# Optimization experiments

Measured on AMD Instinct MI355X. Metric: run time of the kernel, lower is better.

Reference implementation:

```python
import jax, jax.numpy as jnp
import numpy as np

N_NODES = 50000
N_EDGES = 800000
IN_FEATS = 64
HID_FEATS = 64


def _sage_conv(x, src, dst, W_self, W_neigh, b):
    # mean aggregation over in-neighbors (messages flow src -> dst)
    msg_sum = jax.ops.segment_sum(x[src], dst, num_segments=N_NODES)  # [N, d]
    deg = jax.ops.segment_sum(jnp.ones((src.shape[0],), x.dtype), dst,
                              num_segments=N_NODES)  # [N]
    h_neigh = msg_sum / jnp.maximum(deg, 1.0)[:, None]  # zero-degree nodes -> 0
    return x @ W_self + h_neigh @ W_neigh + b


def setup_inputs() -> dict:
    key = jax.random.key(0)
    ks = jax.random.split(key, 12)
    inputs = jax.random.normal(ks[0], (N_NODES, IN_FEATS), dtype=jnp.float32)
    src = jax.random.randint(ks[1], (N_EDGES,), 0, N_NODES, dtype=jnp.int32)
    dst = jax.random.randint(ks[2], (N_EDGES,), 0, N_NODES, dtype=jnp.int32)

    def glorot(k, shape):
        lim = float(np.sqrt(6.0 / (shape[0] + shape[1])))
        return jax.random.uniform(k, shape, jnp.float32, -lim, lim)

    return {
        "inputs": inputs, "src": src, "dst": dst,
        "W_self1": glorot(ks[3], (IN_FEATS, HID_FEATS)),
        "W_neigh1": glorot(ks[4], (IN_FEATS, HID_FEATS)),
        "b1": jnp.zeros((HID_FEATS,), jnp.float32),
        "W_self2": glorot(ks[5], (HID_FEATS, HID_FEATS)),
        "W_neigh2": glorot(ks[6], (HID_FEATS, HID_FEATS)),
        "b2": jnp.zeros((HID_FEATS,), jnp.float32),
        "W_self3": glorot(ks[7], (HID_FEATS, 1)),
        "W_neigh3": glorot(ks[8], (HID_FEATS, 1)),
        "b3": jnp.zeros((1,), jnp.float32),
    }


def reference(inputs, src, dst,
              W_self1, W_neigh1, b1,
              W_self2, W_neigh2, b2,
              W_self3, W_neigh3, b3):
    h = jax.nn.relu(_sage_conv(inputs, src, dst, W_self1, W_neigh1, b1))
    h = jax.nn.relu(_sage_conv(h, src, dst, W_self2, W_neigh2, b2))
    h = _sage_conv(h, src, dst, W_self3, W_neigh3, b3)
    return h  # [N_NODES, 1]
```

## Files before the change

kernel.cpp:

```cpp
#include <hip/hip_runtime.h>

#define N_NODES 50000
#define N_EDGES 800000
#define F 64
#define NTILES (N_NODES / 16)

#define BNODES 128
#define NB ((N_NODES + BNODES - 1) / BNODES)
#define BCAP 2560
#define EPB 2048
#define SCHUNKS ((N_EDGES + EPB - 1) / EPB)
#define SGRID 512
#define SBLOCK 512
#define PREP_ELEMS (4 * F * F + N_NODES * 16)

typedef __attribute__((ext_vector_type(8))) short short8;
typedef __attribute__((ext_vector_type(4))) float f32x4;

union frag16 { uint4 u; short8 s; };


__device__ __forceinline__ float bflo(unsigned int u) {
    union { unsigned int i; float f; } c; c.i = u << 16; return c.f;
}
__device__ __forceinline__ float bfhi(unsigned int u) {
    union { unsigned int i; float f; } c; c.i = u & 0xFFFF0000u; return c.f;
}
__device__ __forceinline__ unsigned short f2bf(float f) {
    union { float f; unsigned int i; } c; c.f = f;
    unsigned int r = c.i + 0x7FFF + ((c.i >> 16) & 1);
    return (unsigned short)(r >> 16);
}


__global__ __launch_bounds__(SBLOCK) void scatter_prep(
        const int* __restrict__ src, const int* __restrict__ dst,
        int* __restrict__ bcur, unsigned int* __restrict__ binned,
        const float* __restrict__ W0, const float* __restrict__ W1,
        const float* __restrict__ W2, const float* __restrict__ W3,
        unsigned short* __restrict__ Wt,
        const float4* __restrict__ xin, ushort4* __restrict__ xout) {
    __shared__ int lcnt[NB];
    __shared__ int scan[SBLOCK];
    __shared__ int gbase[NB];
    __shared__ int lcur[NB];
    __shared__ unsigned int staged[EPB];

    int tid = threadIdx.x;
    int blk = blockIdx.x;

    for (int idx = blk * SBLOCK + tid; idx < PREP_ELEMS; idx += SGRID * SBLOCK) {
        if (idx < 4 * F * F) {
            int m = idx >> 12;
            int e = idx & 4095;
            int n = e >> 6, k = e & 63;
            const float* W = (m == 0) ? W0 : (m == 1) ? W1 : (m == 2) ? W2 : W3;
            Wt[m * F * F + n * F + k] = f2bf(W[k * F + n]);
        } else {
            int i = idx - 4 * F * F;
            float4 v = xin[i];
            ushort4 o;
            o.x = f2bf(v.x); o.y = f2bf(v.y); o.z = f2bf(v.z); o.w = f2bf(v.w);
            xout[i] = o;
        }
    }

    if (blk >= SCHUNKS) return;

    int e0 = blk * EPB;
    int e1 = min(N_EDGES, e0 + EPB);
    for (int i = tid; i < NB; i += SBLOCK) lcnt[i] = 0;
    __syncthreads();

    int dreg[4], sreg[4];
    #pragma unroll
    for (int t = 0; t < 4; ++t) {
        int i = e0 + tid + t * SBLOCK;
        if (i < e1) { dreg[t] = dst[i]; sreg[t] = src[i]; }
        else        { dreg[t] = -1;     sreg[t] = 0; }
    }
    #pragma unroll
    for (int t = 0; t < 4; ++t)
        if (dreg[t] >= 0) atomicAdd(&lcnt[dreg[t] >> 7], 1);
    __syncthreads();

    int v = (tid < NB) ? lcnt[tid] : 0;
    scan[tid] = v;
    __syncthreads();
    for (int off = 1; off < SBLOCK; off <<= 1) {
        int t2 = (tid >= off) ? scan[tid - off] : 0;
        __syncthreads();
        scan[tid] += t2;
        __syncthreads();
    }
    if (tid < NB) {
        int excl = scan[tid] - v;
        int resv = (v > 0) ? atomicAdd(&bcur[tid], v) : 0;
        gbase[tid] = tid * BCAP + resv - excl;
        lcur[tid] = excl;
    }
    __syncthreads();

    #pragma unroll
    for (int t = 0; t < 4; ++t) {
        if (dreg[t] >= 0) {
            int d = dreg[t];
            int b = d >> 7;
            int dl = d & 127;
            int posl = atomicAdd(&lcur[b], 1);
            staged[posl] = (unsigned)sreg[t] | ((unsigned)dl << 16) | ((unsigned)b << 23);
        }
    }
    __syncthreads();

    int cnt = e1 - e0;
    for (int i = tid; i < cnt; i += SBLOCK) {
        unsigned pk = staged[i];
        binned[gbase[pk >> 23] + i] = pk;
    }
}


__global__ __launch_bounds__(512) void bucket_build(
        const unsigned int* __restrict__ binned, const int* __restrict__ bcur,
        int* __restrict__ row_beg, unsigned short* __restrict__ degs,
        unsigned short* __restrict__ csr16) {
    __shared__ int ncnt[BNODES];
    __shared__ int nofs[BNODES];
    __shared__ int ncur[BNODES];
    int blk = blockIdx.x;
    int tid = threadIdx.x;
    int start = blk * BCAP;
    int cnt = min(bcur[blk], BCAP);

    for (int i = tid; i < BNODES; i += 512) ncnt[i] = 0;
    __syncthreads();

    unsigned preg[5];
    #pragma unroll
    for (int t = 0; t < 5; ++t) {
        int i = tid + t * 512;
        preg[t] = (i < cnt) ? binned[start + i] : 0xFFFFFFFFu;
    }
    #pragma unroll
    for (int t = 0; t < 5; ++t)
        if (preg[t] != 0xFFFFFFFFu)
            atomicAdd(&ncnt[(preg[t] >> 16) & 127], 1);
    __syncthreads();

    if (tid < BNODES) nofs[tid] = ncnt[tid];
    __syncthreads();
    for (int off = 1; off < BNODES; off <<= 1) {
        int t2 = (tid >= off && tid < BNODES) ? nofs[tid - off] : 0;
        __syncthreads();
        if (tid < BNODES) nofs[tid] += t2;
        __syncthreads();
    }
    if (tid < BNODES) {
        int excl = nofs[tid] - ncnt[tid];
        ncur[tid] = excl;
        int node = blk * BNODES + tid;
        row_beg[node] = start + excl;
        degs[node] = (unsigned short)ncnt[tid];
    }
    __syncthreads();

    #pragma unroll
    for (int t = 0; t < 5; ++t) {
        if (preg[t] != 0xFFFFFFFFu) {
            unsigned pk = preg[t];
            int dl = (pk >> 16) & 127;
            int pos = start + atomicAdd(&ncur[dl], 1);
            csr16[pos] = (unsigned short)(pk & 0xFFFF);
        }
    }
}


template <bool PROJ>
__global__ __launch_bounds__(256) void aggtf_kernel(
        const uint4* __restrict__ xh8, const int* __restrict__ row_beg,
        const unsigned short* __restrict__ degs,
        const unsigned short* __restrict__ csr16,
        const uint4* __restrict__ Wst, const uint4* __restrict__ Wnt,
        const float* __restrict__ b, unsigned short* __restrict__ out_bf,
        const float* __restrict__ Ws3, const float* __restrict__ Wn3,
        float* __restrict__ pout, float* __restrict__ qout) {
    __shared__ uint4 lagg[16 * 8];
    int tid  = threadIdx.x;
    int wave = tid >> 6;
    int lane = tid & 63;
    int base = blockIdx.x * 16;

    int g   = lane >> 3;
    int sub = lane & 7;

    int rb_l = 0, dg_l = 0;
    if (lane < 16) { rb_l = row_beg[base + lane]; dg_l = degs[base + lane]; }

    for (int nl = wave * 4; nl < wave * 4 + 4; ++nl) {
        int beg = __shfl(rb_l, nl);
        int deg = __shfl(dg_l, nl);
        int end = beg + deg;
        float a0[8], a1[8];
        #pragma unroll
        for (int j = 0; j < 8; ++j) { a0[j] = 0.f; a1[j] = 0.f; }
        int i = beg + g;
        for (; i + 8 < end; i += 16) {
            int i0 = csr16[i];
            int i1 = csr16[i + 8];
            uint4 v0 = xh8[i0 * 8 + sub];
            uint4 v1 = xh8[i1 * 8 + sub];
            a0[0] += bflo(v0.x); a0[1] += bfhi(v0.x); a0[2] += bflo(v0.y); a0[3] += bfhi(v0.y);
            a0[4] += bflo(v0.z); a0[5] += bfhi(v0.z); a0[6] += bflo(v0.w); a0[7] += bfhi(v0.w);
            a1[0] += bflo(v1.x); a1[1] += bfhi(v1.x); a1[2] += bflo(v1.y); a1[3] += bfhi(v1.y);
            a1[4] += bflo(v1.z); a1[5] += bfhi(v1.z); a1[6] += bflo(v1.w); a1[7] += bfhi(v1.w);
        }
        if (i < end) {
            uint4 v0 = xh8[csr16[i] * 8 + sub];
            a0[0] += bflo(v0.x); a0[1] += bfhi(v0.x); a0[2] += bflo(v0.y); a0[3] += bfhi(v0.y);
            a0[4] += bflo(v0.z); a0[5] += bfhi(v0.z); a0[6] += bflo(v0.w); a0[7] += bfhi(v0.w);
        }
        float s[8];
        #pragma unroll
        for (int j = 0; j < 8; ++j) s[j] = a0[j] + a1[j];
        #pragma unroll
        for (int off = 8; off <= 32; off <<= 1)
            #pragma unroll
            for (int j = 0; j < 8; ++j)
                s[j] += __shfl_xor(s[j], off);
        if (g == 0) {
            float inv = (deg > 0) ? (1.0f / (float)deg) : 0.f;
            unsigned short o[8];
            #pragma unroll
            for (int j = 0; j < 8; ++j) o[j] = f2bf(s[j] * inv);
            uint4 pk;
            pk.x = (unsigned)o[0] | ((unsigned)o[1] << 16);
            pk.y = (unsigned)o[2] | ((unsigned)o[3] << 16);
            pk.z = (unsigned)o[4] | ((unsigned)o[5] << 16);
            pk.w = (unsigned)o[6] | ((unsigned)o[7] << 16);
            lagg[nl * 8 + sub] = pk;
        }
    }
    __syncthreads();
    if (wave != 0) return;

    int lo = lane & 15, hi = lane >> 4;

    frag16 ws[2][4], wn[2][4];
    #pragma unroll
    for (int kt = 0; kt < 2; ++kt)
        #pragma unroll
        for (int jt = 0; jt < 4; ++jt) {
            int n = jt * 16 + lo;
            ws[kt][jt].u = Wst[n * 8 + kt * 4 + hi];
            wn[kt][jt].u = Wnt[n * 8 + kt * 4 + hi];
        }
    float bias_s[4];
    #pragma unroll
    for (int jt = 0; jt < 4; ++jt) bias_s[jt] = b[jt * 16 + lo];
    float w3n_s[4], w3s_s[4];
    if constexpr (PROJ) {
        #pragma unroll
        for (int jt = 0; jt < 4; ++jt) {
            w3n_s[jt] = Wn3[jt * 16 + lo];
            w3s_s[jt] = Ws3[jt * 16 + lo];
        }
    }

    frag16 ax[2], aa[2];
    #pragma unroll
    for (int kt = 0; kt < 2; ++kt) {
        ax[kt].u = xh8[(base + lo) * 8 + kt * 4 + hi];
        aa[kt].u = lagg[lo * 8 + kt * 4 + hi];
    }

    f32x4 acc[4];
    #pragma unroll
    for (int jt = 0; jt < 4; ++jt)
        acc[jt] = f32x4{bias_s[jt], bias_s[jt], bias_s[jt], bias_s[jt]};

    #pragma unroll
    for (int kt = 0; kt < 2; ++kt)
        #pragma unroll
        for (int jt = 0; jt < 4; ++jt) {
            acc[jt] = __builtin_amdgcn_mfma_f32_16x16x32_bf16(ax[kt].s, ws[kt][jt].s, acc[jt], 0, 0, 0);
            acc[jt] = __builtin_amdgcn_mfma_f32_16x16x32_bf16(aa[kt].s, wn[kt][jt].s, acc[jt], 0, 0, 0);
        }

    if constexpr (!PROJ) {
        #pragma unroll
        for (int jt = 0; jt < 4; ++jt)
            #pragma unroll
            for (int r = 0; r < 4; ++r) {
                float h = fmaxf(acc[jt][r], 0.f);
                out_bf[(base + hi * 4 + r) * F + jt * 16 + lo] = f2bf(h);
            }
    } else {
        #pragma unroll
        for (int r = 0; r < 4; ++r) {
            float pr = 0.f, qr = 0.f;
            #pragma unroll
            for (int jt = 0; jt < 4; ++jt) {
                float h = fmaxf(acc[jt][r], 0.f);
                pr += h * w3n_s[jt];
                qr += h * w3s_s[jt];
            }
            #pragma unroll
            for (int off = 1; off < 16; off <<= 1) {
                pr += __shfl_xor(pr, off);
                qr += __shfl_xor(qr, off);
            }
            if (lo == 0) {
                pout[base + hi * 4 + r] = pr;
                qout[base + hi * 4 + r] = qr;
            }
        }
    }
}


__global__ __launch_bounds__(256) void final_kernel(
        const int* __restrict__ row_beg, const unsigned short* __restrict__ degs,
        const unsigned short* __restrict__ csr16,
        const float* __restrict__ p, const float* __restrict__ q,
        const float* __restrict__ b3, float* __restrict__ out, int n_nodes) {
    int grp = threadIdx.x >> 4;
    int ln  = threadIdx.x & 15;
    int node = blockIdx.x * 16 + grp;
    if (node >= n_nodes) return;
    int beg = row_beg[node];
    int deg = degs[node];
    int end = beg + deg;
    float s = 0.f;
    for (int i = beg + ln; i < end; i += 16) s += p[csr16[i]];
    #pragma unroll
    for (int off = 1; off < 16; off <<= 1) s += __shfl_xor(s, off);
    if (ln == 0) {
        float inv = (deg > 0) ? (1.0f / (float)deg) : 0.f;
        out[node] = q[node] + s * inv + b3[0];
    }
}


extern "C" void kernel_launch(void* const* d_in, const int* in_sizes, int n_in,
                              void* d_out, int out_size, void* d_ws, size_t ws_size,
                              hipStream_t stream) {
    const float* x   = (const float*)d_in[0];
    const int*   src = (const int*)d_in[1];
    const int*   dst = (const int*)d_in[2];
    const float* Ws1 = (const float*)d_in[3];
    const float* Wn1 = (const float*)d_in[4];
    const float* b1  = (const float*)d_in[5];
    const float* Ws2 = (const float*)d_in[6];
    const float* Wn2 = (const float*)d_in[7];
    const float* b2  = (const float*)d_in[8];
    const float* Ws3 = (const float*)d_in[9];
    const float* Wn3 = (const float*)d_in[10];
    const float* b3  = (const float*)d_in[11];
    float* out = (float*)d_out;

    char* ws = (char*)d_ws;
    size_t cur = 0;
    auto alloc = [&](size_t bytes) -> void* {
        void* ptr = ws + cur;
        cur += (bytes + 255) & ~(size_t)255;
        return ptr;
    };

    int*            bcur     = (int*)  alloc(NB * sizeof(int));
    unsigned int*   binned   = (unsigned int*)alloc((size_t)NB * BCAP * sizeof(unsigned int));
    int*            row_beg  = (int*)  alloc((size_t)(NB * BNODES) * sizeof(int));
    unsigned short* degs     = (unsigned short*)alloc((size_t)(NB * BNODES) * sizeof(unsigned short));
    unsigned short* csr16    = (unsigned short*)alloc((size_t)NB * BCAP * sizeof(unsigned short));
    unsigned short* xh       = (unsigned short*)alloc((size_t)N_NODES * F * 2);
    unsigned short* h1h      = (unsigned short*)alloc((size_t)N_NODES * F * 2);
    unsigned short* Wt       = (unsigned short*)alloc(4 * F * F * 2);
    float*          p        = (float*)alloc(N_NODES * sizeof(float));
    float*          q        = (float*)alloc(N_NODES * sizeof(float));

    unsigned short* Wst1 = Wt;
    unsigned short* Wnt1 = Wt + F * F;
    unsigned short* Wst2 = Wt + 2 * F * F;
    unsigned short* Wnt2 = Wt + 3 * F * F;

    (void)hipMemsetAsync(bcur, 0, NB * sizeof(int), stream);
    scatter_prep<<<SGRID, SBLOCK, 0, stream>>>(
        src, dst, bcur, binned, Ws1, Wn1, Ws2, Wn2, Wt, (const float4*)x, (ushort4*)xh);
    bucket_build<<<NB, 512, 0, stream>>>(binned, bcur, row_beg, degs, csr16);

    aggtf_kernel<false><<<NTILES, 256, 0, stream>>>(
        (const uint4*)xh, row_beg, degs, csr16,
        (const uint4*)Wst1, (const uint4*)Wnt1, b1, h1h,
        nullptr, nullptr, nullptr, nullptr);
    aggtf_kernel<true><<<NTILES, 256, 0, stream>>>(
        (const uint4*)h1h, row_beg, degs, csr16,
        (const uint4*)Wst2, (const uint4*)Wnt2, b2, nullptr,
        Ws3, Wn3, p, q);
    final_kernel<<<(N_NODES + 15) / 16, 256, 0, stream>>>(
        row_beg, degs, csr16, p, q, b3, out, N_NODES);
}
```

Before: 167.9 us.

## Assign one node per 8-lane group in aggregation, 32 nodes per block

The gather-aggregate phase is remapped. Each 8-lane group now walks one node's full edge list on its own, so a 256-thread block covers 32 nodes, where before a wave spread each node's edges across all 8 groups and then did cross-lane shuffle reductions. This removes the shuffle reductions and the sequential per-wave node loop, and two waves then run the MFMA transform on 16-node halves. The trade-off is a longer serial dependence chain per lane and divergence from uneven degrees within a wave.

```diff
diff --git a/kernel.cpp b/kernel.cpp
--- a/kernel.cpp
+++ b/kernel.cpp
@@ -4,6 +4,7 @@
 #define N_EDGES 800000
 #define F 64
 #define NTILES (N_NODES / 16)
+#define ATILES ((N_NODES + 31) / 32)
 
 #define BNODES 128
 #define NB ((N_NODES + BNODES - 1) / BNODES)
@@ -186,64 +187,62 @@
         const float* __restrict__ b, unsigned short* __restrict__ out_bf,
         const float* __restrict__ Ws3, const float* __restrict__ Wn3,
         float* __restrict__ pout, float* __restrict__ qout) {
-    __shared__ uint4 lagg[16 * 8];
+    __shared__ uint4 lagg[32 * 8];
     int tid  = threadIdx.x;
     int wave = tid >> 6;
     int lane = tid & 63;
-    int base = blockIdx.x * 16;
-
-    int g   = lane >> 3;
-    int sub = lane & 7;
+    int base = blockIdx.x * 32;
+
+    int nsub = lane >> 3;
+    int sub  = lane & 7;
+    int node_l = wave * 8 + nsub;
 
     int rb_l = 0, dg_l = 0;
-    if (lane < 16) { rb_l = row_beg[base + lane]; dg_l = degs[base + lane]; }
-
-    for (int nl = wave * 4; nl < wave * 4 + 4; ++nl) {
-        int beg = __shfl(rb_l, nl);
-        int deg = __shfl(dg_l, nl);
-        int end = beg + deg;
-        float a0[8], a1[8];
-        #pragma unroll
-        for (int j = 0; j < 8; ++j) { a0[j] = 0.f; a1[j] = 0.f; }
-        int i = beg + g;
-        for (; i + 8 < end; i += 16) {
-            int i0 = csr16[i];
-            int i1 = csr16[i + 8];
-            uint4 v0 = xh8[i0 * 8 + sub];
-            uint4 v1 = xh8[i1 * 8 + sub];
-            a0[0] += bflo(v0.x); a0[1] += bfhi(v0.x); a0[2] += bflo(v0.y); a0[3] += bfhi(v0.y);
-            a0[4] += bflo(v0.z); a0[5] += bfhi(v0.z); a0[6] += bflo(v0.w); a0[7] += bfhi(v0.w);
-            a1[0] += bflo(v1.x); a1[1] += bfhi(v1.x); a1[2] += bflo(v1.y); a1[3] += bfhi(v1.y);
-            a1[4] += bflo(v1.z); a1[5] += bfhi(v1.z); a1[6] += bflo(v1.w); a1[7] += bfhi(v1.w);
-        }
-        if (i < end) {
-            uint4 v0 = xh8[csr16[i] * 8 + sub];
-            a0[0] += bflo(v0.x); a0[1] += bfhi(v0.x); a0[2] += bflo(v0.y); a0[3] += bfhi(v0.y);
-            a0[4] += bflo(v0.z); a0[5] += bfhi(v0.z); a0[6] += bflo(v0.w); a0[7] += bfhi(v0.w);
-        }
-        float s[8];
-        #pragma unroll
-        for (int j = 0; j < 8; ++j) s[j] = a0[j] + a1[j];
-        #pragma unroll
-        for (int off = 8; off <= 32; off <<= 1)
-            #pragma unroll
-            for (int j = 0; j < 8; ++j)
-                s[j] += __shfl_xor(s[j], off);
-        if (g == 0) {
-            float inv = (deg > 0) ? (1.0f / (float)deg) : 0.f;
-            unsigned short o[8];
-            #pragma unroll
-            for (int j = 0; j < 8; ++j) o[j] = f2bf(s[j] * inv);
-            uint4 pk;
-            pk.x = (unsigned)o[0] | ((unsigned)o[1] << 16);
-            pk.y = (unsigned)o[2] | ((unsigned)o[3] << 16);
-            pk.z = (unsigned)o[4] | ((unsigned)o[5] << 16);
-            pk.w = (unsigned)o[6] | ((unsigned)o[7] << 16);
-            lagg[nl * 8 + sub] = pk;
-        }
-    }
-    __syncthreads();
-    if (wave != 0) return;
+    if (lane < 32 && base + lane < N_NODES) {
+        rb_l = row_beg[base + lane];
+        dg_l = degs[base + lane];
+    }
+    int beg = __shfl(rb_l, node_l);
+    int deg = __shfl(dg_l, node_l);
+    int end = beg + deg;
+
+    float a0[8], a1[8];
+    #pragma unroll
+    for (int j = 0; j < 8; ++j) { a0[j] = 0.f; a1[j] = 0.f; }
+
+    int i = beg;
+    for (; i + 1 < end; i += 2) {
+        int i0 = csr16[i];
+        int i1 = csr16[i + 1];
+        uint4 v0 = xh8[i0 * 8 + sub];
+        uint4 v1 = xh8[i1 * 8 + sub];
+        a0[0] += bflo(v0.x); a0[1] += bfhi(v0.x); a0[2] += bflo(v0.y); a0[3] += bfhi(v0.y);
+        a0[4] += bflo(v0.z); a0[5] += bfhi(v0.z); a0[6] += bflo(v0.w); a0[7] += bfhi(v0.w);
+        a1[0] += bflo(v1.x); a1[1] += bfhi(v1.x); a1[2] += bflo(v1.y); a1[3] += bfhi(v1.y);
+        a1[4] += bflo(v1.z); a1[5] += bfhi(v1.z); a1[6] += bflo(v1.w); a1[7] += bfhi(v1.w);
+    }
+    if (i < end) {
+        uint4 v0 = xh8[csr16[i] * 8 + sub];
+        a0[0] += bflo(v0.x); a0[1] += bfhi(v0.x); a0[2] += bflo(v0.y); a0[3] += bfhi(v0.y);
+        a0[4] += bflo(v0.z); a0[5] += bfhi(v0.z); a0[6] += bflo(v0.w); a0[7] += bfhi(v0.w);
+    }
+    {
+        float inv = (deg > 0) ? (1.0f / (float)deg) : 0.f;
+        unsigned short o[8];
+        #pragma unroll
+        for (int j = 0; j < 8; ++j) o[j] = f2bf((a0[j] + a1[j]) * inv);
+        uint4 pk;
+        pk.x = (unsigned)o[0] | ((unsigned)o[1] << 16);
+        pk.y = (unsigned)o[2] | ((unsigned)o[3] << 16);
+        pk.z = (unsigned)o[4] | ((unsigned)o[5] << 16);
+        pk.w = (unsigned)o[6] | ((unsigned)o[7] << 16);
+        lagg[node_l * 8 + sub] = pk;
+    }
+    __syncthreads();
+
+    if (wave >= 2) return;
+    int tbase = base + wave * 16;
+    if (tbase + 16 > N_NODES) return;
 
     int lo = lane & 15, hi = lane >> 4;
 
@@ -271,8 +270,8 @@
     frag16 ax[2], aa[2];
     #pragma unroll
     for (int kt = 0; kt < 2; ++kt) {
-        ax[kt].u = xh8[(base + lo) * 8 + kt * 4 + hi];
-        aa[kt].u = lagg[lo * 8 + kt * 4 + hi];
+        ax[kt].u = xh8[(tbase + lo) * 8 + kt * 4 + hi];
+        aa[kt].u = lagg[(wave * 16 + lo) * 8 + kt * 4 + hi];
     }
 
     f32x4 acc[4];
@@ -294,7 +293,7 @@
             #pragma unroll
             for (int r = 0; r < 4; ++r) {
                 float h = fmaxf(acc[jt][r], 0.f);
-                out_bf[(base + hi * 4 + r) * F + jt * 16 + lo] = f2bf(h);
+                out_bf[(tbase + hi * 4 + r) * F + jt * 16 + lo] = f2bf(h);
             }
     } else {
         #pragma unroll
@@ -312,8 +311,8 @@
                 qr += __shfl_xor(qr, off);
             }
             if (lo == 0) {
-                pout[base + hi * 4 + r] = pr;
-                qout[base + hi * 4 + r] = qr;
+                pout[tbase + hi * 4 + r] = pr;
+                qout[tbase + hi * 4 + r] = qr;
             }
         }
     }
@@ -389,11 +388,11 @@
         src, dst, bcur, binned, Ws1, Wn1, Ws2, Wn2, Wt, (const float4*)x, (ushort4*)xh);
     bucket_build<<<NB, 512, 0, stream>>>(binned, bcur, row_beg, degs, csr16);
 
-    aggtf_kernel<false><<<NTILES, 256, 0, stream>>>(
+    aggtf_kernel<false><<<ATILES, 256, 0, stream>>>(
         (const uint4*)xh, row_beg, degs, csr16,
         (const uint4*)Wst1, (const uint4*)Wnt1, b1, h1h,
         nullptr, nullptr, nullptr, nullptr);
-    aggtf_kernel<true><<<NTILES, 256, 0, stream>>>(
+    aggtf_kernel<true><<<ATILES, 256, 0, stream>>>(
         (const uint4*)h1h, row_beg, degs, csr16,
         (const uint4*)Wst2, (const uint4*)Wnt2, b2, nullptr,
         Ws3, Wn3, p, q);
```

New measurement: 160.5 us. -4.4%, faster.
